# Optimization experiments

Measured on AMD Instinct MI355X. Metric: run time of the kernel, lower is better.

Reference implementation:

```python
import jax, jax.numpy as jnp
import numpy as np

VOCAB, D, MAX_LEN = 32000, 256, 128
BATCH, SEQ = 32, 128


def setup_inputs() -> dict:
    key = jax.random.key(0)
    ks = jax.random.split(key, 8)
    s = 1.0 / np.sqrt(D)  # torch nn.Linear default init scale
    X = jax.random.randint(ks[0], (BATCH, SEQ), 0, VOCAB)
    emb = jax.random.normal(ks[1], (VOCAB, D), dtype=jnp.float32)
    W_l = jax.random.uniform(ks[2], (D, D), minval=-s, maxval=s, dtype=jnp.float32)
    b_l = jax.random.uniform(ks[3], (D,), minval=-s, maxval=s, dtype=jnp.float32)
    W_r = jax.random.uniform(ks[4], (D, D), minval=-s, maxval=s, dtype=jnp.float32)
    b_r = jax.random.uniform(ks[5], (D,), minval=-s, maxval=s, dtype=jnp.float32)
    W_rn = jax.random.uniform(ks[6], (D, D), minval=-s, maxval=s, dtype=jnp.float32)
    b_rn = jax.random.uniform(ks[7], (D,), minval=-s, maxval=s, dtype=jnp.float32)
    return {"X": X, "emb": emb, "W_l": W_l, "b_l": b_l,
            "W_r": W_r, "b_r": b_r, "W_rn": W_rn, "b_rn": b_rn}


def reference(X, emb, W_l, b_l, W_r, b_r, W_rn, b_rn):
    X = X[:, :MAX_LEN]
    n = X.shape[1]
    Xe = emb[X]                               # (B, n, D) embedding lookup
    Xl = Xe @ W_l.T + b_l                     # (B, n, D)
    Xr = Xe @ W_r.T + b_r                     # (B, n, D)
    # pairwise: pair[b, i, j] = relu(Xl[b, j] + Xr[b, i])  -> (B, n, n, D)
    pair = jax.nn.relu(Xl[:, None, :, :] + Xr[:, :, None, :])
    # linear_rn then sum over (i, j); by linearity: sum(pair) @ W_rn.T + n^2 * b_rn
    pooled = pair.sum(axis=(1, 2))            # (B, D)
    return pooled @ W_rn.T + (n * n) * b_rn   # (B, D)
```

## Files before the change

kernel.cpp:

```cpp
#include <hip/hip_runtime.h>

#define D 256
#define S 128
#define B 32

typedef __attribute__((ext_vector_type(8))) short bf16x8;
typedef __attribute__((ext_vector_type(4))) float f32x4;

__device__ __forceinline__ unsigned short f2bf(float f) {
    union { float f; unsigned u; } v; v.f = f;
    unsigned r = v.u + 0x7FFFu + ((v.u >> 16) & 1u);
    return (unsigned short)(r >> 16);
}
__device__ __forceinline__ float dot4(float4 a, float4 b) {
    return a.x * b.x + a.y * b.y + a.z * b.z + a.w * b.w;
}
__device__ __forceinline__ bf16x8 pack8(const float4 f0, const float4 f1) {
    union { unsigned short u[8]; bf16x8 v; } r;
    r.u[0] = f2bf(f0.x); r.u[1] = f2bf(f0.y); r.u[2] = f2bf(f0.z); r.u[3] = f2bf(f0.w);
    r.u[4] = f2bf(f1.x); r.u[5] = f2bf(f1.y); r.u[6] = f2bf(f1.z); r.u[7] = f2bf(f1.w);
    return r.v;
}

__global__ __launch_bounds__(256) void k0_cast(
    const float* __restrict__ Wl, const float* __restrict__ Wr,
    unsigned short* __restrict__ Wb)
{
    const int idx = blockIdx.x * 256 + threadIdx.x;
    const int e = idx * 4;
    const int n = e >> 8, k = e & 255;
    const float* src = (n < 256) ? (Wl + (size_t)n * D + k)
                                 : (Wr + (size_t)(n - 256) * D + k);
    const float4 f = *(const float4*)src;
    ushort4 h;
    h.x = f2bf(f.x); h.y = f2bf(f.y); h.z = f2bf(f.z); h.w = f2bf(f.w);
    *(ushort4*)(Wb + (size_t)n * D + k) = h;
}

__global__ __launch_bounds__(256) void k12_fused(
    const int* __restrict__ X, const float* __restrict__ emb,
    const unsigned short* __restrict__ Wb,
    const float* __restrict__ bl, const float* __restrict__ br,
    float* __restrict__ pooled)
{
    constexpr int LP = 17;
    __shared__ float lxl[S * LP];
    __shared__ float lxr[S * LP];
    __shared__ float red[256];

    const int b   = blockIdx.x & 31;
    const int dc  = blockIdx.x >> 5;
    const int tid = threadIdx.x;
    const int w   = tid >> 6;
    const int l   = tid & 63;
    const int lm  = l & 15;
    const int lq  = l >> 4;

    const int r0 = w * 32 + lm;
    const int tok0 = X[b * S + r0];
    const int tok1 = X[b * S + r0 + 16];
    const float* a0 = emb + (size_t)tok0 * D;
    const float* a1 = emb + (size_t)tok1 * D;
    const unsigned short* bp_l = Wb + (size_t)(dc * 16 + lm) * D + lq * 8;
    const unsigned short* bp_r = bp_l + (size_t)256 * D;

    f32x4 acc[2][2];
#pragma unroll
    for (int rt = 0; rt < 2; ++rt)
#pragma unroll
        for (int ct = 0; ct < 2; ++ct)
            acc[rt][ct] = (f32x4){0.f, 0.f, 0.f, 0.f};

#pragma unroll
    for (int ks = 0; ks < 8; ++ks) {
        const int k0 = ks * 32 + lq * 8;
        const bf16x8 af0 = pack8(*(const float4*)(a0 + k0),
                                 *(const float4*)(a0 + k0 + 4));
        const bf16x8 af1 = pack8(*(const float4*)(a1 + k0),
                                 *(const float4*)(a1 + k0 + 4));
        const bf16x8 bf_l = *(const bf16x8*)(bp_l + ks * 32);
        const bf16x8 bf_r = *(const bf16x8*)(bp_r + ks * 32);
        acc[0][0] = __builtin_amdgcn_mfma_f32_16x16x32_bf16(af0, bf_l, acc[0][0], 0, 0, 0);
        acc[0][1] = __builtin_amdgcn_mfma_f32_16x16x32_bf16(af0, bf_r, acc[0][1], 0, 0, 0);
        acc[1][0] = __builtin_amdgcn_mfma_f32_16x16x32_bf16(af1, bf_l, acc[1][0], 0, 0, 0);
        acc[1][1] = __builtin_amdgcn_mfma_f32_16x16x32_bf16(af1, bf_r, acc[1][1], 0, 0, 0);
    }

    {
        const float bvl = bl[dc * 16 + lm];
        const float bvr = br[dc * 16 + lm];
#pragma unroll
        for (int rt = 0; rt < 2; ++rt) {
#pragma unroll
            for (int i = 0; i < 4; ++i) {
                const int row = w * 32 + rt * 16 + lq * 4 + i;
                lxl[row * LP + lm] = acc[rt][0][i] + bvl;
                lxr[row * LP + lm] = acc[rt][1][i] + bvr;
            }
        }
    }
    __syncthreads();

    const int dl = tid & 15;
    const int ig = tid >> 4;

    float xr[8];
    float sr = 0.f;
#pragma unroll
    for (int u = 0; u < 8; ++u) {
        xr[u] = lxr[(ig * 8 + u) * LP + dl];
        sr += xr[u];
    }

    float sa[8];
#pragma unroll
    for (int u = 0; u < 8; ++u) sa[u] = 0.f;
    float sxl = 0.f;
#pragma unroll 4
    for (int j = 0; j < S; ++j) {
        const float x = lxl[j * LP + dl];
        sxl += x;
#pragma unroll
        for (int u = 0; u < 8; ++u)
            sa[u] += fabsf(x + xr[u]);
    }
    float sabs = ((sa[0] + sa[1]) + (sa[2] + sa[3]))
               + ((sa[4] + sa[5]) + (sa[6] + sa[7]));

    red[tid] = sabs + (float)S * sr;
    __syncthreads();

    if (tid < 16) {
        float tot = 0.f;
#pragma unroll
        for (int g = 0; g < 16; ++g) tot += red[g * 16 + tid];
        pooled[(size_t)b * D + (size_t)dc * 16 + tid] =
            0.5f * ((float)S * sxl + tot);
    }
}

__global__ __launch_bounds__(256) void k3_out(
    const float* __restrict__ pooled, const float* __restrict__ Wrn,
    const float* __restrict__ brn, float* __restrict__ out)
{
    __shared__ float lp[D];
    __shared__ float red[256];
    const int bb = blockIdx.x >> 3;
    const int dc = blockIdx.x & 7;
    const int tid = threadIdx.x;
    lp[tid] = pooled[(size_t)bb * D + tid];
    __syncthreads();

    const int dl = tid & 31;
    const int kg = tid >> 5;
    const int d = dc * 32 + dl;
    const float4* __restrict__ w4 = (const float4*)(Wrn + (size_t)d * D) + kg * 8;
    const float4* __restrict__ p4 = (const float4*)lp + kg * 8;
    float acc = 0.f;
#pragma unroll
    for (int f = 0; f < 8; ++f) acc += dot4(w4[f], p4[f]);

    red[tid] = acc;
    __syncthreads();
    if (tid < 32) {
        float s = 0.f;
#pragma unroll
        for (int g = 0; g < 8; ++g) s += red[g * 32 + tid];
        out[(size_t)bb * D + dc * 32 + tid] = s + (float)(S * S) * brn[dc * 32 + tid];
    }
}

extern "C" void kernel_launch(void* const* d_in, const int* in_sizes, int n_in,
                              void* d_out, int out_size, void* d_ws, size_t ws_size,
                              hipStream_t stream) {
    const int*   X   = (const int*)d_in[0];
    const float* emb = (const float*)d_in[1];
    const float* Wl  = (const float*)d_in[2];
    const float* bl  = (const float*)d_in[3];
    const float* Wr  = (const float*)d_in[4];
    const float* br  = (const float*)d_in[5];
    const float* Wrn = (const float*)d_in[6];
    const float* brn = (const float*)d_in[7];
    float* out = (float*)d_out;

    unsigned short* Wb = (unsigned short*)d_ws;
    float* pooled = (float*)(Wb + (size_t)512 * D);

    k0_cast<<<128, 256, 0, stream>>>(Wl, Wr, Wb);
    k12_fused<<<B * (D / 16), 256, 0, stream>>>(X, emb, Wb, bl, br, pooled);
    k3_out<<<B * 8, 256, 0, stream>>>(pooled, Wrn, brn, out);
}
```

Measured before the change: 110.4 us.

## Drop weight cast kernel, convert fp32 weights inline, and run output GEMV in place

```diff
diff --git a/kernel.cpp b/kernel.cpp
--- a/kernel.cpp
+++ b/kernel.cpp
@@ -22,24 +22,9 @@
     return r.v;
 }
 
-__global__ __launch_bounds__(256) void k0_cast(
-    const float* __restrict__ Wl, const float* __restrict__ Wr,
-    unsigned short* __restrict__ Wb)
-{
-    const int idx = blockIdx.x * 256 + threadIdx.x;
-    const int e = idx * 4;
-    const int n = e >> 8, k = e & 255;
-    const float* src = (n < 256) ? (Wl + (size_t)n * D + k)
-                                 : (Wr + (size_t)(n - 256) * D + k);
-    const float4 f = *(const float4*)src;
-    ushort4 h;
-    h.x = f2bf(f.x); h.y = f2bf(f.y); h.z = f2bf(f.z); h.w = f2bf(f.w);
-    *(ushort4*)(Wb + (size_t)n * D + k) = h;
-}
-
 __global__ __launch_bounds__(256) void k12_fused(
     const int* __restrict__ X, const float* __restrict__ emb,
-    const unsigned short* __restrict__ Wb,
+    const float* __restrict__ Wl, const float* __restrict__ Wr,
     const float* __restrict__ bl, const float* __restrict__ br,
     float* __restrict__ pooled)
 {
@@ -61,8 +46,8 @@
     const int tok1 = X[b * S + r0 + 16];
     const float* a0 = emb + (size_t)tok0 * D;
     const float* a1 = emb + (size_t)tok1 * D;
-    const unsigned short* bp_l = Wb + (size_t)(dc * 16 + lm) * D + lq * 8;
-    const unsigned short* bp_r = bp_l + (size_t)256 * D;
+    const float* bp_l = Wl + (size_t)(dc * 16 + lm) * D + lq * 8;
+    const float* bp_r = Wr + (size_t)(dc * 16 + lm) * D + lq * 8;
 
     f32x4 acc[2][2];
 #pragma unroll
@@ -78,8 +63,10 @@
                                  *(const float4*)(a0 + k0 + 4));
         const bf16x8 af1 = pack8(*(const float4*)(a1 + k0),
                                  *(const float4*)(a1 + k0 + 4));
-        const bf16x8 bf_l = *(const bf16x8*)(bp_l + ks * 32);
-        const bf16x8 bf_r = *(const bf16x8*)(bp_r + ks * 32);
+        const bf16x8 bf_l = pack8(*(const float4*)(bp_l + ks * 32),
+                                  *(const float4*)(bp_l + ks * 32 + 4));
+        const bf16x8 bf_r = pack8(*(const float4*)(bp_r + ks * 32),
+                                  *(const float4*)(bp_r + ks * 32 + 4));
         acc[0][0] = __builtin_amdgcn_mfma_f32_16x16x32_bf16(af0, bf_l, acc[0][0], 0, 0, 0);
         acc[0][1] = __builtin_amdgcn_mfma_f32_16x16x32_bf16(af0, bf_r, acc[0][1], 0, 0, 0);
         acc[1][0] = __builtin_amdgcn_mfma_f32_16x16x32_bf16(af1, bf_l, acc[1][0], 0, 0, 0);
@@ -139,35 +126,23 @@
     }
 }
 
-__global__ __launch_bounds__(256) void k3_out(
-    const float* __restrict__ pooled, const float* __restrict__ Wrn,
-    const float* __restrict__ brn, float* __restrict__ out)
+__global__ __launch_bounds__(256) void k3_inplace(
+    float* __restrict__ io, const float* __restrict__ Wrn,
+    const float* __restrict__ brn)
 {
     __shared__ float lp[D];
-    __shared__ float red[256];
-    const int bb = blockIdx.x >> 3;
-    const int dc = blockIdx.x & 7;
+    const int bb  = blockIdx.x;
     const int tid = threadIdx.x;
-    lp[tid] = pooled[(size_t)bb * D + tid];
+    lp[tid] = io[(size_t)bb * D + tid];
     __syncthreads();
 
-    const int dl = tid & 31;
-    const int kg = tid >> 5;
-    const int d = dc * 32 + dl;
-    const float4* __restrict__ w4 = (const float4*)(Wrn + (size_t)d * D) + kg * 8;
-    const float4* __restrict__ p4 = (const float4*)lp + kg * 8;
+    const float4* __restrict__ w4 = (const float4*)(Wrn + (size_t)tid * D);
+    const float4* __restrict__ p4 = (const float4*)lp;
     float acc = 0.f;
-#pragma unroll
-    for (int f = 0; f < 8; ++f) acc += dot4(w4[f], p4[f]);
+#pragma unroll 16
+    for (int f = 0; f < 64; ++f) acc += dot4(w4[f], p4[f]);
 
-    red[tid] = acc;
-    __syncthreads();
-    if (tid < 32) {
-        float s = 0.f;
-#pragma unroll
-        for (int g = 0; g < 8; ++g) s += red[g * 32 + tid];
-        out[(size_t)bb * D + dc * 32 + tid] = s + (float)(S * S) * brn[dc * 32 + tid];
-    }
+    io[(size_t)bb * D + tid] = acc + (float)(S * S) * brn[tid];
 }
 
 extern "C" void kernel_launch(void* const* d_in, const int* in_sizes, int n_in,
@@ -183,10 +158,6 @@
     const float* brn = (const float*)d_in[7];
     float* out = (float*)d_out;
 
-    unsigned short* Wb = (unsigned short*)d_ws;
-    float* pooled = (float*)(Wb + (size_t)512 * D);
-
-    k0_cast<<<128, 256, 0, stream>>>(Wl, Wr, Wb);
-    k12_fused<<<B * (D / 16), 256, 0, stream>>>(X, emb, Wb, bl, br, pooled);
-    k3_out<<<B * 8, 256, 0, stream>>>(pooled, Wrn, brn, out);
+    k12_fused<<<B * (D / 16), 256, 0, stream>>>(X, emb, Wl, Wr, bl, br, out);
+    k3_inplace<<<B, 256, 0, stream>>>(out, Wrn, brn);
 }
```

After: 120.6 us. 1.09x slower.
